# Kernel tuning notes

Measured on AMD Instinct MI355X. Metric: run time of the kernel, lower is better.

## Reference

```python
import jax, jax.numpy as jnp
import numpy as np

HEADS = 8
LN_EPS = 1e-5
BN_EPS = 1e-5
MIN_EPS, MAX_EPS = 1e-4, 10.0


def _ln(x, g, b):
    m = x.mean(-1, keepdims=True)
    v = x.var(-1, keepdims=True)
    return (x - m) / jnp.sqrt(v + LN_EPS) * g + b


def _pos2d(a, b, dim, temperature=10000.0):
    # faithful to build_2d_sincos_position_embedding(w=a, h=b)
    grid_a = jnp.arange(a, dtype=jnp.float32)
    grid_b = jnp.arange(b, dtype=jnp.float32)
    ga, gb = jnp.meshgrid(grid_a, grid_b, indexing='ij')  # (a, b)
    pos_dim = dim // 4
    omega = 1.0 / (temperature ** (jnp.arange(pos_dim, dtype=jnp.float32) / pos_dim))
    out_a = ga.flatten()[:, None] * omega[None]
    out_b = gb.flatten()[:, None] * omega[None]
    return jnp.concatenate([jnp.sin(out_a), jnp.cos(out_a), jnp.sin(out_b), jnp.cos(out_b)], axis=1)  # (a*b, dim)


def _avgpool(x, k):
    bb, cc, H, W = x.shape
    return x.reshape(bb, cc, H // k, k, W // k, k).mean((3, 5))


def setup_inputs() -> dict:
    key = jax.random.key(0)
    c1, c2, bs = 256, 512, 16
    ks = jax.random.split(key, 12)

    def lin(k, o, i):
        return (jax.random.normal(k, (o, i), jnp.float32) * (1.0 / np.sqrt(i))).astype(jnp.float32)

    return {
        'a3': jax.random.normal(ks[0], (bs, c1, 80, 80), jnp.float32),
        'a4': jax.random.normal(ks[1], (bs, c2, 40, 40), jnp.float32),
        'conv_w': lin(ks[2], c1, c2), 'conv_b': jnp.zeros((c1,), jnp.float32),
        'bn_g': jnp.ones((c1,), jnp.float32), 'bn_b': jnp.zeros((c1,), jnp.float32),
        'q_w': lin(ks[3], c1, c1), 'q_b': jnp.zeros((c1,), jnp.float32),
        'q_ln_g': jnp.ones((c1,), jnp.float32), 'q_ln_b': jnp.zeros((c1,), jnp.float32),
        'k_w': lin(ks[4], c1, c1), 'k_b': jnp.zeros((c1,), jnp.float32),
        'k_ln_g': jnp.ones((c1,), jnp.float32), 'k_ln_b': jnp.zeros((c1,), jnp.float32),
        'v_w': lin(ks[5], c1, c1), 'v_b': jnp.zeros((c1,), jnp.float32),
        'out_w': lin(ks[6], c1, c1), 'out_b': jnp.zeros((c1,), jnp.float32),
        'lin1_w': lin(ks[7], 4 * c1, c1), 'lin1_b': jnp.zeros((4 * c1,), jnp.float32),
        'lin2_w': lin(ks[8], c1, 4 * c1), 'lin2_b': jnp.zeros((c1,), jnp.float32),
        'norm1_g': jnp.ones((c1,), jnp.float32), 'norm1_b': jnp.zeros((c1,), jnp.float32),
        'norm2_g': jnp.ones((c1,), jnp.float32), 'norm2_b': jnp.zeros((c1,), jnp.float32),
        'idx': 10,
    }


def reference(a3, a4, conv_w, conv_b, bn_g, bn_b, q_w, q_b, q_ln_g, q_ln_b,
              k_w, k_b, k_ln_g, k_ln_b, v_w, v_b, out_w, out_b,
              lin1_w, lin1_b, lin2_w, lin2_b, norm1_g, norm1_b, norm2_g, norm2_b, idx):
    a3 = jnp.nan_to_num(a3, nan=0.0, posinf=1e4, neginf=-1e4)
    a4 = jnp.nan_to_num(a4, nan=0.0, posinf=1e4, neginf=-1e4)
    orig_a3, orig_a4 = a3, a4

    # high_to_low_embed: 1x1 conv + BatchNorm (eval: running_mean=0, running_var=1)
    a4e = jnp.einsum('bchw,oc->bohw', a4, conv_w) + conv_b[None, :, None, None]
    a4e = a4e / jnp.sqrt(1.0 + BN_EPS) * bn_g[None, :, None, None] + bn_b[None, :, None, None]

    if idx == 10:
        a3d = _avgpool(a3, 2)
    else:
        a3d = _avgpool(a3, 4)
        a4e = _avgpool(a4e, 2)

    bs, c, h, w = a3d.shape
    tgt = h * w
    src = a4e.shape[2] * a4e.shape[3]

    residual = a3d.reshape(bs, c, tgt).transpose(0, 2, 1)      # (bs, tgt, c)
    a3f = a3d.reshape(bs, c, tgt).transpose(2, 0, 1)            # (tgt, bs, c)
    a4f = a4e.reshape(bs, c, src).transpose(2, 0, 1)            # (src, bs, c)

    pos = _pos2d(h, w, c)[:, None, :]                           # (h*w, 1, c)
    a3f = a3f + pos
    a4f = a4f + pos                                             # src == tgt by construction

    Q = jax.nn.relu(_ln(a3f @ q_w.T + q_b, q_ln_g, q_ln_b))
    K = jax.nn.relu(_ln(a4f @ k_w.T + k_b, k_ln_g, k_ln_b))
    V = a4f @ v_w.T + v_b

    hd = c // HEADS
    Q = Q.reshape(tgt, bs, HEADS, hd).transpose(1, 2, 0, 3)     # (b, h, tgt, hd)
    K = K.reshape(src, bs, HEADS, hd).transpose(1, 2, 0, 3)
    V = V.reshape(src, bs, HEADS, hd).transpose(1, 2, 0, 3)

    m = max(src, tgt)
    wi = (np.pi / 2) * jnp.arange(1, m + 1, dtype=jnp.float32) / m  # (m,)
    sq = jnp.sin(wi[:tgt])[None, None, :, None]
    cq = jnp.cos(wi[:tgt])[None, None, :, None]
    sk = jnp.sin(wi[:src])[None, None, :, None]
    ck = jnp.cos(wi[:src])[None, None, :, None]
    Q_ = jnp.concatenate([Q * sq, Q * cq], -1)                  # (b, h, tgt, 2hd)
    K_ = jnp.concatenate([K * sk, K * ck], -1)                  # (b, h, src, 2hd)

    KV = jnp.einsum('bhsd,bhse->bhde', K_, V)                   # (b, h, 2hd, hd)
    Zden = jnp.einsum('bhld,bhd->bhl', Q_, K_.sum(2))
    Z = 1.0 / jnp.clip(Zden, MIN_EPS, MAX_EPS)
    attn = jnp.einsum('bhld,bhde->bhle', Q_, KV) * Z[..., None]  # (b, h, tgt, hd)

    attn = attn.transpose(2, 0, 1, 3).reshape(tgt, bs, c)
    out = (attn @ out_w.T + out_b).transpose(1, 0, 2)           # (bs, tgt, c)
    out = _ln(out, norm1_g, norm1_b)
    out = residual + out

    res2 = out
    ff = jax.nn.gelu(out @ lin1_w.T + lin1_b, approximate=False) @ lin2_w.T + lin2_b
    ff = _ln(ff, norm2_g, norm2_b)
    out = res2 + ff

    a3_sa = out.transpose(0, 2, 1).reshape(bs, c, h, w)
    a3_sa = jax.image.resize(a3_sa, orig_a3.shape, 'bilinear')  # align_corners=False
    a3_sa = a3_sa * orig_a3

    B4, C4, H4, W4 = orig_a4.shape
    a4_up = jax.image.resize(orig_a4, (B4, C4, 2 * H4, 2 * W4), 'bilinear')
    return (a3_sa, a4_up)
```

## Files before the change

### kernel.cpp

```cpp
#include <hip/hip_runtime.h>
#include <math.h>


typedef __attribute__((ext_vector_type(8))) short bf16x8;
typedef __attribute__((ext_vector_type(8))) unsigned short us8;
typedef __attribute__((ext_vector_type(4))) unsigned short us4h;
typedef __attribute__((ext_vector_type(4))) float f32x4;

__device__ __forceinline__ unsigned short f2bf(float f) {
  unsigned int u = __float_as_uint(f);
  u += 0x7fff + ((u >> 16) & 1);
  return (unsigned short)(u >> 16);
}
__device__ __forceinline__ float bf2f(unsigned short u) {
  return __uint_as_float(((unsigned int)u) << 16);
}

__device__ __forceinline__ void gload16(const void* g, void* l) {
  __builtin_amdgcn_global_load_lds(
      (const __attribute__((address_space(1))) void*)g,
      (__attribute__((address_space(3))) void*)l, 16, 0, 0);
}

__global__ __launch_bounds__(256) void prep_kernel(
    const float* __restrict__ cw, const float* __restrict__ qw,
    const float* __restrict__ kw, const float* __restrict__ vw,
    const float* __restrict__ ow, const float* __restrict__ l1w,
    const float* __restrict__ l2w, unsigned short* __restrict__ wbf,
    float* __restrict__ pos) {
  if (blockIdx.x < 448) {
    int gid = blockIdx.x * 256 + threadIdx.x;
    size_t e0 = (size_t)gid * 8;
    const float* src; size_t off;
    if (e0 < 131072)      { src = cw;  off = e0; }
    else if (e0 < 196608) { src = qw;  off = e0 - 131072; }
    else if (e0 < 262144) { src = kw;  off = e0 - 196608; }
    else if (e0 < 327680) { src = vw;  off = e0 - 262144; }
    else if (e0 < 393216) { src = ow;  off = e0 - 327680; }
    else if (e0 < 655360) { src = l1w; off = e0 - 393216; }
    else                  { src = l2w; off = e0 - 655360; }
    float4 v0 = *(const float4*)(src + off);
    float4 v1 = *(const float4*)(src + off + 4);
    us8 r;
    r[0] = f2bf(v0.x); r[1] = f2bf(v0.y); r[2] = f2bf(v0.z); r[3] = f2bf(v0.w);
    r[4] = f2bf(v1.x); r[5] = f2bf(v1.y); r[6] = f2bf(v1.z); r[7] = f2bf(v1.w);
    *(us8*)(wbf + e0) = r;
  } else {
    int s = blockIdx.x - 448, c = threadIdx.x;
    int y = s / 40, x = s - y * 40;
    int quad = c >> 6, i = c & 63;
    float omega = expf(-(float)i * (9.2103403719761836f / 64.0f));
    float coord = (quad < 2) ? (float)y : (float)x;
    float a = coord * omega;
    pos[s * 256 + c] = (quad & 1) ? cosf(a) : sinf(a);
  }
}

__global__ __launch_bounds__(640) void avgpool_kernel(
    const float* __restrict__ a3, const float* __restrict__ pos,
    unsigned short* __restrict__ X3) {
  __shared__ float buf2[256][44];
  int y = blockIdx.x, b = blockIdx.y;
  int tid = threadIdx.x;
  int x2 = tid % 20, cq = tid / 20;
#pragma unroll
  for (int it = 0; it < 8; ++it) {
    int c = cq + 32 * it;
    const float* p = a3 + (((size_t)(b * 256 + c) * 80 + 2 * y) * 80 + x2 * 4);
    float4 r0 = *(const float4*)p;
    float4 r1 = *(const float4*)(p + 80);
    buf2[c][2 * x2]     = 0.25f * ((r0.x + r0.y) + (r1.x + r1.y));
    buf2[c][2 * x2 + 1] = 0.25f * ((r0.z + r0.w) + (r1.z + r1.w));
  }
  __syncthreads();
  size_t t0 = (size_t)b * 1600 + y * 40;
  int sbase = y * 40;
#pragma unroll
  for (int it = 0; it < 4; ++it) {
    int idx = it * 640 + tid;
    int c = idx & 255, xq = idx >> 8;
    int x0 = xq * 4;
    float4 v = *(const float4*)&buf2[c][x0];
#pragma unroll
    for (int j = 0; j < 4; ++j) {
      float pv = pos[(size_t)(sbase + x0 + j) * 256 + c];
      float vv = (j == 0) ? v.x : (j == 1) ? v.y : (j == 2) ? v.z : v.w;
      X3[(t0 + x0 + j) * 256 + c] = f2bf(vv + pv);
    }
  }
}

__global__ __launch_bounds__(256) void a4t_kernel(
    const float* __restrict__ a4, unsigned short* __restrict__ a4t) {
  __shared__ float buf[64][65];
  int s0 = blockIdx.x * 64, k0 = blockIdx.y * 64, b = blockIdx.z;
  const float* src = a4 + ((size_t)b * 512 + k0) * 1600 + s0;
#pragma unroll
  for (int p = 0; p < 4; ++p) {
    int idx = p * 256 + threadIdx.x;
    int kk = idx >> 4, s4 = (idx & 15) * 4;
    float4 v = *(const float4*)(src + (size_t)kk * 1600 + s4);
    buf[kk][s4 + 0] = v.x; buf[kk][s4 + 1] = v.y;
    buf[kk][s4 + 2] = v.z; buf[kk][s4 + 3] = v.w;
  }
  __syncthreads();
  unsigned short* dst = a4t + ((size_t)b * 1600 + s0) * 512 + k0;
#pragma unroll
  for (int p = 0; p < 4; ++p) {
    int idx = p * 256 + threadIdx.x;
    int ss = idx >> 4, kq = (idx & 15) * 4;
    us4h v;
    v[0] = f2bf(buf[kq + 0][ss]); v[1] = f2bf(buf[kq + 1][ss]);
    v[2] = f2bf(buf[kq + 2][ss]); v[3] = f2bf(buf[kq + 3][ss]);
    *(us4h*)(dst + (size_t)ss * 512 + kq) = v;
  }
}

struct __align__(16) SmemT {
  unsigned short Albs[64][32];
  unsigned short Wlds[256][32];
  float part[4][64][2];
};

template<int EPI>
__device__ __forceinline__ void gemm_body(
    SmemT& S,
    const unsigned short* __restrict__ A, const unsigned short* __restrict__ W,
    const float* __restrict__ bias, void* __restrict__ outp,
    const int K, const int ldN, int t0, int o0,
    const float* __restrict__ posb,
    const float* __restrict__ g1, const float* __restrict__ b1,
    const unsigned short* __restrict__ res) {
  int tid = threadIdx.x;
  int lane = tid & 63, w = tid >> 6;
  int mw = w >> 2, nw = w & 3;
  int g = lane >> 4, cl = lane & 15;
  f32x4 acc[2][4] = {};

  int arow = lane >> 2, acol = (lane & 3) * 8;
  const unsigned short* ag  = A + (size_t)(t0 + (w & 3) * 16 + arow) * K + acol;
  const unsigned short* wgA = W + (size_t)(o0 + w * 16 + arow) * K + acol;
  const unsigned short* wgB = W + (size_t)(o0 + 128 + w * 16 + arow) * K + acol;
  unsigned short* al  = &S.Albs[(w & 3) * 16][0];
  unsigned short* wlA = &S.Wlds[w * 16][0];
  unsigned short* wlB = &S.Wlds[128 + w * 16][0];

  for (int k0 = 0; k0 < K; k0 += 32) {
    __syncthreads();
    if (w < 4) gload16(ag + k0, al);
    gload16(wgA + k0, wlA);
    gload16(wgB + k0, wlB);
    __syncthreads();
    bf16x8 af[2], bw[4];
#pragma unroll
    for (int ms = 0; ms < 2; ++ms)
      af[ms] = *(const bf16x8*)&S.Albs[mw * 32 + ms * 16 + cl][g * 8];
#pragma unroll
    for (int ns = 0; ns < 4; ++ns)
      bw[ns] = *(const bf16x8*)&S.Wlds[nw * 64 + ns * 16 + cl][g * 8];
#pragma unroll
    for (int ms = 0; ms < 2; ++ms)
#pragma unroll
      for (int ns = 0; ns < 4; ++ns)
        acc[ms][ns] = __builtin_amdgcn_mfma_f32_16x16x32_bf16(af[ms], bw[ns], acc[ms][ns], 0, 0, 0);
  }

  float bv[4];
#pragma unroll
  for (int ns = 0; ns < 4; ++ns) bv[ns] = bias[o0 + nw * 64 + ns * 16 + cl];
  int sbase = t0 % 1600;

  if constexpr (EPI == 2 || EPI == 3 || EPI == 5) {
#pragma unroll
    for (int ms = 0; ms < 2; ++ms) {
#pragma unroll
      for (int i = 0; i < 4; ++i) {
        float p = 0.f, q = 0.f;
#pragma unroll
        for (int ns = 0; ns < 4; ++ns) {
          float v = acc[ms][ns][i] + bv[ns];
          p += v; q += v * v;
        }
        p += __shfl_xor(p, 1); q += __shfl_xor(q, 1);
        p += __shfl_xor(p, 2); q += __shfl_xor(q, 2);
        p += __shfl_xor(p, 4); q += __shfl_xor(q, 4);
        p += __shfl_xor(p, 8); q += __shfl_xor(q, 8);
        if (cl == 0) {
          int rl = mw * 32 + ms * 16 + g * 4 + i;
          S.part[nw][rl][0] = p;
          S.part[nw][rl][1] = q;
        }
      }
    }
    __syncthreads();
  }

  if constexpr (EPI == 5) {
    float* of = (float*)outp;
    int bb = t0 / 1600;
#pragma unroll
    for (int ms = 0; ms < 2; ++ms) {
      int rl0 = mw * 32 + ms * 16 + g * 4;
      float mean[4], inv[4];
#pragma unroll
      for (int i = 0; i < 4; ++i) {
        float sp = (S.part[0][rl0 + i][0] + S.part[1][rl0 + i][0]) +
                   (S.part[2][rl0 + i][0] + S.part[3][rl0 + i][0]);
        float sq = (S.part[0][rl0 + i][1] + S.part[1][rl0 + i][1]) +
                   (S.part[2][rl0 + i][1] + S.part[3][rl0 + i][1]);
        mean[i] = sp * (1.f / 256.f);
        float var = sq * (1.f / 256.f) - mean[i] * mean[i];
        inv[i] = rsqrtf(var + 1e-5f);
      }
#pragma unroll
      for (int ns = 0; ns < 4; ++ns) {
        int col = nw * 64 + ns * 16 + cl;
        float gg = g1[col], b2 = b1[col];
        float4 y;
#pragma unroll
        for (int i = 0; i < 4; ++i) {
          float v = acc[ms][ns][i] + bv[ns];
          float yy = (v - mean[i]) * inv[i] * gg + b2;
          yy += bf2f(res[(size_t)(t0 + rl0 + i) * 256 + col]);
          if (i == 0) y.x = yy; else if (i == 1) y.y = yy;
          else if (i == 2) y.z = yy; else y.w = yy;
        }
        *(float4*)(of + ((size_t)(bb * 256 + col) * 1600) + sbase + rl0) = y;
      }
    }
    return;
  }

  unsigned short* ob = (unsigned short*)outp;
#pragma unroll
  for (int ms = 0; ms < 2; ++ms) {
#pragma unroll
    for (int i = 0; i < 4; ++i) {
      int rl = mw * 32 + ms * 16 + g * 4 + i;
      int t = t0 + rl;
      float mean = 0.f, inv = 0.f;
      if constexpr (EPI == 2 || EPI == 3) {
        float sp = (S.part[0][rl][0] + S.part[1][rl][0]) + (S.part[2][rl][0] + S.part[3][rl][0]);
        float sq = (S.part[0][rl][1] + S.part[1][rl][1]) + (S.part[2][rl][1] + S.part[3][rl][1]);
        mean = sp * (1.f / 256.f);
        float var = sq * (1.f / 256.f) - mean * mean;
        inv = rsqrtf(var + 1e-5f);
      }
#pragma unroll
      for (int ns = 0; ns < 4; ++ns) {
        int col = nw * 64 + ns * 16 + cl;
        float v = acc[ms][ns][i] + bv[ns];
        size_t oidx = (size_t)t * ldN + o0 + col;
        if constexpr (EPI == 0) {
          ob[oidx] = f2bf(v);
        } else if constexpr (EPI == 1) {
          const float is = 0.99999500003749968f;
          float y = v * (is * g1[col]) + b1[col] + posb[(size_t)(sbase + rl) * 256 + col];
          ob[oidx] = f2bf(y);
        } else if constexpr (EPI == 2) {
          float y = (v - mean) * inv * g1[col] + b1[col];
          ob[oidx] = f2bf(fmaxf(y, 0.f));
        } else if constexpr (EPI == 3) {
          float y = (v - mean) * inv * g1[col] + b1[col];
          y += bf2f(res[(size_t)t * 256 + col]) - posb[(size_t)(sbase + rl) * 256 + col];
          ob[oidx] = f2bf(y);
        } else if constexpr (EPI == 4) {
          float y = 0.5f * v * (1.f + erff(v * 0.7071067811865475f));
          ob[oidx] = f2bf(y);
        }
      }
    }
  }
}

template<int EPI>
__global__ __launch_bounds__(512) void fgemm(
    const unsigned short* __restrict__ A, const unsigned short* __restrict__ W,
    const float* __restrict__ bias, void* __restrict__ outp,
    const int K, const int ldN,
    const float* __restrict__ posb,
    const float* __restrict__ g1, const float* __restrict__ b1,
    const unsigned short* __restrict__ res) {
  __shared__ SmemT S;
  gemm_body<EPI>(S, A, W, bias, outp, K, ldN, blockIdx.x * 64, blockIdx.y * 256,
                 posb, g1, b1, res);
}

__global__ __launch_bounds__(512) void qkv_kernel(
    const unsigned short* __restrict__ X3b, const unsigned short* __restrict__ X4b,
    const unsigned short* __restrict__ w_q, const unsigned short* __restrict__ w_k,
    const unsigned short* __restrict__ w_v,
    const float* __restrict__ q_b, const float* __restrict__ k_b, const float* __restrict__ v_b,
    const float* __restrict__ q_g, const float* __restrict__ q_bt,
    const float* __restrict__ k_g, const float* __restrict__ k_bt,
    unsigned short* __restrict__ Qo, unsigned short* __restrict__ Ko,
    unsigned short* __restrict__ Vo) {
  __shared__ SmemT S;
  int t0 = blockIdx.x * 64;
  if (blockIdx.y == 0) {
    gemm_body<2>(S, X3b, w_q, q_b, Qo, 256, 256, t0, 0, nullptr, q_g, q_bt, nullptr);
  } else if (blockIdx.y == 1) {
    gemm_body<2>(S, X4b, w_k, k_b, Ko, 256, 256, t0, 0, nullptr, k_g, k_bt, nullptr);
  } else {
    gemm_body<0>(S, X4b, w_v, v_b, Vo, 256, 256, t0, 0, nullptr, nullptr, nullptr, nullptr);
  }
}

__global__ __launch_bounds__(256) void kv_kernel(
    const unsigned short* __restrict__ Kb, const unsigned short* __restrict__ Vb,
    float* __restrict__ KVp, float* __restrict__ Ksp) {
  __shared__ float Kc[64][32];
  __shared__ float Vc[64][32];
  __shared__ float sv[64], cv[64];
  __shared__ float red[4][64];
  int bx = blockIdx.x;
  int bh = bx / 5, sp = bx - bh * 5;
  int b = bh >> 3, h = bh & 7;
  int tid = threadIdx.x;
  int e = tid & 31, dg = tid >> 5;
  int d4 = dg * 4;
  int dks = tid & 63, partid = tid >> 6;
  float accs[4] = {0.f, 0.f, 0.f, 0.f};
  float accc[4] = {0.f, 0.f, 0.f, 0.f};
  float ks = 0.f;
  size_t base = ((size_t)b * 1600) * 256 + h * 32;
  for (int s0 = sp * 320; s0 < sp * 320 + 320; s0 += 64) {
    __syncthreads();
#pragma unroll
    for (int p = 0; p < 8; ++p) {
      int si = dg + p * 8;
      Kc[si][e] = bf2f(Kb[base + (size_t)(s0 + si) * 256 + e]);
      Vc[si][e] = bf2f(Vb[base + (size_t)(s0 + si) * 256 + e]);
    }
    if (tid < 64) {
      float wv = 1.5707963267948966f * (float)(s0 + tid + 1) * (1.0f / 1600.0f);
      sv[tid] = sinf(wv);
      cv[tid] = cosf(wv);
    }
    __syncthreads();
#pragma unroll 8
    for (int si = 0; si < 64; ++si) {
      float vv = Vc[si][e];
      float sn = sv[si], cs = cv[si];
      float4 k4 = *(const float4*)&Kc[si][d4];
      float p0 = k4.x * vv, p1 = k4.y * vv, p2 = k4.z * vv, p3 = k4.w * vv;
      accs[0] = fmaf(p0, sn, accs[0]); accc[0] = fmaf(p0, cs, accc[0]);
      accs[1] = fmaf(p1, sn, accs[1]); accc[1] = fmaf(p1, cs, accc[1]);
      accs[2] = fmaf(p2, sn, accs[2]); accc[2] = fmaf(p2, cs, accc[2]);
      accs[3] = fmaf(p3, sn, accs[3]); accc[3] = fmaf(p3, cs, accc[3]);
    }
#pragma unroll 4
    for (int q = 0; q < 16; ++q) {
      int si = partid * 16 + q;
      float kvv = (dks < 32) ? Kc[si][dks] * sv[si] : Kc[si][dks - 32] * cv[si];
      ks += kvv;
    }
  }
  red[partid][dks] = ks;
  __syncthreads();
  size_t ob = (size_t)sp * 128 + bh;
  if (tid < 64)
    Ksp[ob * 64 + tid] = (red[0][tid] + red[1][tid]) + (red[2][tid] + red[3][tid]);
#pragma unroll
  for (int i = 0; i < 4; ++i) {
    KVp[ob * 2048 + (d4 + i) * 32 + e] = accs[i];
    KVp[ob * 2048 + (32 + d4 + i) * 32 + e] = accc[i];
  }
}

__global__ __launch_bounds__(256) void kvred_kernel(
    const float* __restrict__ KVp, const float* __restrict__ Ksp,
    float* __restrict__ KV, float* __restrict__ Ks) {
  int bh = blockIdx.x, tid = threadIdx.x;
  size_t o = (size_t)bh * 2048 + tid * 8;
  float4 s0 = make_float4(0, 0, 0, 0), s1 = make_float4(0, 0, 0, 0);
#pragma unroll
  for (int sp = 0; sp < 5; ++sp) {
    const float* p = KVp + ((size_t)sp * 128 + bh) * 2048 + tid * 8;
    float4 a = *(const float4*)p;
    float4 b2 = *(const float4*)(p + 4);
    s0.x += a.x; s0.y += a.y; s0.z += a.z; s0.w += a.w;
    s1.x += b2.x; s1.y += b2.y; s1.z += b2.z; s1.w += b2.w;
  }
  *(float4*)(KV + o) = s0;
  *(float4*)(KV + o + 4) = s1;
  if (tid < 64) {
    float t = 0.f;
#pragma unroll
    for (int sp = 0; sp < 5; ++sp) t += Ksp[((size_t)sp * 128 + bh) * 64 + tid];
    Ks[bh * 64 + tid] = t;
  }
}

__global__ __launch_bounds__(256) void attn_kernel(
    const unsigned short* __restrict__ Qb, const float* __restrict__ KV,
    const float* __restrict__ Ksum, unsigned short* __restrict__ attn) {
  int grp = threadIdx.x >> 5;
  int e = threadIdx.x & 31;
  int t = blockIdx.x * 8 + grp;
  int b = t / 1600, s = t - b * 1600;
  float wv = 1.5707963267948966f * (float)(s + 1) * (1.0f / 1600.0f);
  float sq = sinf(wv), cq = cosf(wv);
  const unsigned short* qrow = Qb + (size_t)t * 256;
  for (int h = 0; h < 8; ++h) {
    int bh = b * 8 + h;
    const float* kv = KV + (size_t)bh * 2048;
    const float* ksm = Ksum + (size_t)bh * 64;
    float qe = bf2f(qrow[h * 32 + e]);
    float zp = qe * (sq * ksm[e] + cq * ksm[32 + e]);
    zp += __shfl_xor(zp, 1); zp += __shfl_xor(zp, 2);
    zp += __shfl_xor(zp, 4); zp += __shfl_xor(zp, 8); zp += __shfl_xor(zp, 16);
    float acc = 0.f;
#pragma unroll 8
    for (int d = 0; d < 32; ++d) {
      float qv = bf2f(qrow[h * 32 + d]);
      acc = fmaf(qv * sq, kv[d * 32 + e], acc);
      acc = fmaf(qv * cq, kv[(32 + d) * 32 + e], acc);
    }
    float zc = fminf(fmaxf(zp, 1e-4f), 10.0f);
    attn[(size_t)t * 256 + h * 32 + e] = f2bf(acc * (1.0f / zc));
  }
}

__device__ __forceinline__ float4 up_row4(const float* sm, int Y, int q) {
  float fy = Y * 0.5f - 0.25f;
  int iy = (int)floorf(fy);
  float dy = fy - (float)iy;
  int y0 = iy < 0 ? 0 : iy;
  int y1 = (iy + 1) > 39 ? 39 : (iy + 1);
  const float* r0 = sm + y0 * 40;
  const float* r1 = sm + y1 * 40;
  int cm1 = (2 * q - 1) < 0 ? 0 : (2 * q - 1);
  int cp2 = (2 * q + 2) > 39 ? 39 : (2 * q + 2);
  float w1 = 1.f - dy;
  float s0 = w1 * r0[cm1]       + dy * r1[cm1];
  float s1 = w1 * r0[2 * q]     + dy * r1[2 * q];
  float s2 = w1 * r0[2 * q + 1] + dy * r1[2 * q + 1];
  float s3 = w1 * r0[cp2]       + dy * r1[cp2];
  float4 o;
  o.x = 0.25f * s0 + 0.75f * s1;
  o.y = 0.75f * s1 + 0.25f * s2;
  o.z = 0.25f * s1 + 0.75f * s2;
  o.w = 0.75f * s2 + 0.25f * s3;
  return o;
}

__global__ __launch_bounds__(256) void upsample_fused_kernel(
    const float* __restrict__ a3p, const float* __restrict__ a3,
    const float* __restrict__ a4, float* __restrict__ out0,
    float* __restrict__ out1) {
  __shared__ float sm[1600];
  int id = blockIdx.x;
  const float* src;
  float* outp;
  const float* mul = nullptr;
  if (id < 4096) {
    int c = id & 255, b = id >> 8;
    src = a3p + ((size_t)b * 256 + c) * 1600;
    outp = out0 + ((size_t)b * 256 + c) * 6400;
    mul = a3 + ((size_t)b * 256 + c) * 6400;
  } else {
    int id2 = id - 4096;
    int c = id2 & 511, b = id2 >> 9;
    src = a4 + ((size_t)b * 512 + c) * 1600;
    outp = out1 + ((size_t)b * 512 + c) * 6400;
  }
  for (int i = threadIdx.x; i < 400; i += 256)
    *(float4*)&sm[i * 4] = *(const float4*)(src + i * 4);
  __syncthreads();
  if (mul) {
    for (int i = threadIdx.x; i < 1600; i += 256) {
      int Y = i / 20, q = i - Y * 20;
      float4 o = up_row4(sm, Y, q);
      float4 m = *(const float4*)(mul + i * 4);
      o.x *= m.x; o.y *= m.y; o.z *= m.z; o.w *= m.w;
      *(float4*)(outp + i * 4) = o;
    }
  } else {
    for (int i = threadIdx.x; i < 1600; i += 256) {
      int Y = i / 20, q = i - Y * 20;
      float4 o = up_row4(sm, Y, q);
      *(float4*)(outp + i * 4) = o;
    }
  }
}

extern "C" void kernel_launch(void* const* d_in, const int* in_sizes, int n_in,
                              void* d_out, int out_size, void* d_ws, size_t ws_size,
                              hipStream_t stream) {
  const float* a3     = (const float*)d_in[0];
  const float* a4     = (const float*)d_in[1];
  const float* conv_w = (const float*)d_in[2];
  const float* conv_b = (const float*)d_in[3];
  const float* bn_g   = (const float*)d_in[4];
  const float* bn_b   = (const float*)d_in[5];
  const float* q_w    = (const float*)d_in[6];
  const float* q_b    = (const float*)d_in[7];
  const float* q_ln_g = (const float*)d_in[8];
  const float* q_ln_b = (const float*)d_in[9];
  const float* k_w    = (const float*)d_in[10];
  const float* k_b    = (const float*)d_in[11];
  const float* k_ln_g = (const float*)d_in[12];
  const float* k_ln_b = (const float*)d_in[13];
  const float* v_w    = (const float*)d_in[14];
  const float* v_b    = (const float*)d_in[15];
  const float* out_w  = (const float*)d_in[16];
  const float* out_b  = (const float*)d_in[17];
  const float* lin1_w = (const float*)d_in[18];
  const float* lin1_b = (const float*)d_in[19];
  const float* lin2_w = (const float*)d_in[20];
  const float* lin2_b = (const float*)d_in[21];
  const float* n1_g   = (const float*)d_in[22];
  const float* n1_b   = (const float*)d_in[23];
  const float* n2_g   = (const float*)d_in[24];
  const float* n2_b   = (const float*)d_in[25];
  (void)in_sizes; (void)n_in; (void)out_size; (void)ws_size;

  float* ws = (float*)d_ws;
  float* pos  = ws + 0;
  unsigned short* wbf = (unsigned short*)(ws + 409600);
  float* KV   = ws + 868352;
  float* Ks   = ws + 1130496;
  float* KVp  = ws + 1138688;
  float* Ksp  = ws + 2449408;
  unsigned short* X3b  = (unsigned short*)(ws + 2490368);
  unsigned short* X4b  = (unsigned short*)(ws + 5767168);
  unsigned short* Qbb  = (unsigned short*)(ws + 9043968);
  unsigned short* Kbb  = (unsigned short*)(ws + 12320768);
  unsigned short* Vbb  = (unsigned short*)(ws + 15597568);
  unsigned short* o1b  = (unsigned short*)(ws + 18874368);
  unsigned short* a4tb = (unsigned short*)(ws + 22151168);
  unsigned short* ffhb = (unsigned short*)(ws + 22151168);
  float* a3p  = ws + 9043968;

  const unsigned short* w_conv = wbf;
  const unsigned short* w_q    = wbf + 131072;
  const unsigned short* w_k    = wbf + 196608;
  const unsigned short* w_v    = wbf + 262144;
  const unsigned short* w_o    = wbf + 327680;
  const unsigned short* w_l1   = wbf + 393216;
  const unsigned short* w_l2   = wbf + 655360;

  float* out0 = (float*)d_out;
  float* out1f = out0 + (size_t)16 * 256 * 80 * 80;

  prep_kernel<<<2048, 256, 0, stream>>>(conv_w, q_w, k_w, v_w, out_w, lin1_w, lin2_w, wbf, pos);
  avgpool_kernel<<<dim3(40, 16), 640, 0, stream>>>(a3, pos, X3b);
  a4t_kernel<<<dim3(25, 8, 16), 256, 0, stream>>>(a4, a4tb);
  fgemm<1><<<dim3(400, 1), 512, 0, stream>>>(a4tb, w_conv, conv_b, X4b, 512, 256, pos, bn_g, bn_b, nullptr);
  qkv_kernel<<<dim3(400, 3), 512, 0, stream>>>(X3b, X4b, w_q, w_k, w_v,
      q_b, k_b, v_b, q_ln_g, q_ln_b, k_ln_g, k_ln_b, Qbb, Kbb, Vbb);
  kv_kernel<<<640, 256, 0, stream>>>(Kbb, Vbb, KVp, Ksp);
  kvred_kernel<<<128, 256, 0, stream>>>(KVp, Ksp, KV, Ks);
  attn_kernel<<<3200, 256, 0, stream>>>(Qbb, KV, Ks, Kbb );
  fgemm<3><<<dim3(400, 1), 512, 0, stream>>>(Kbb, w_o, out_b, o1b, 256, 256, pos, n1_g, n1_b, X3b);
  fgemm<4><<<dim3(400, 4), 512, 0, stream>>>(o1b, w_l1, lin1_b, ffhb, 256, 1024, nullptr, nullptr, nullptr, nullptr);
  fgemm<5><<<dim3(400, 1), 512, 0, stream>>>(ffhb, w_l2, lin2_b, a3p, 1024, 256, nullptr, n2_g, n2_b, o1b);
  upsample_fused_kernel<<<12288, 256, 0, stream>>>(a3p, a3, a4, out0, out1f);
}
```

Baseline: 385.6 us.

## Merge a4 transpose into prep kernel and widen GEMM K-step to 64

The a4 transpose-to-bf16 work moves into the prep kernel as extra blocks, which removes one kernel launch. The shared GEMM body now loads a 64-wide K slab per iteration into two 32-wide LDS buffers, with all 8 waves sharing the loads. Each slab feeds two MFMA sub-steps, which halves the number of barrier pairs per tile. In exchange, LDS use per block doubles and the prep kernel now reserves a 64x65 float shared buffer on every block, which could lower occupancy.

```diff
diff --git a/kernel.cpp b/kernel.cpp
--- a/kernel.cpp
+++ b/kernel.cpp
@@ -27,7 +27,9 @@
     const float* __restrict__ kw, const float* __restrict__ vw,
     const float* __restrict__ ow, const float* __restrict__ l1w,
     const float* __restrict__ l2w, unsigned short* __restrict__ wbf,
-    float* __restrict__ pos) {
+    float* __restrict__ pos,
+    const float* __restrict__ a4, unsigned short* __restrict__ a4t) {
+  __shared__ float buf[64][65];
   if (blockIdx.x < 448) {
     int gid = blockIdx.x * 256 + threadIdx.x;
     size_t e0 = (size_t)gid * 8;
@@ -45,7 +47,7 @@
     r[0] = f2bf(v0.x); r[1] = f2bf(v0.y); r[2] = f2bf(v0.z); r[3] = f2bf(v0.w);
     r[4] = f2bf(v1.x); r[5] = f2bf(v1.y); r[6] = f2bf(v1.z); r[7] = f2bf(v1.w);
     *(us8*)(wbf + e0) = r;
-  } else {
+  } else if (blockIdx.x < 2048) {
     int s = blockIdx.x - 448, c = threadIdx.x;
     int y = s / 40, x = s - y * 40;
     int quad = c >> 6, i = c & 63;
@@ -53,6 +55,31 @@
     float coord = (quad < 2) ? (float)y : (float)x;
     float a = coord * omega;
     pos[s * 256 + c] = (quad & 1) ? cosf(a) : sinf(a);
+  } else {
+    int id = blockIdx.x - 2048;
+    int b = id / 200;
+    int r = id - b * 200;
+    int s0 = (r % 25) * 64, k0 = (r / 25) * 64;
+    const float* src = a4 + ((size_t)b * 512 + k0) * 1600 + s0;
+#pragma unroll
+    for (int p = 0; p < 4; ++p) {
+      int idx = p * 256 + threadIdx.x;
+      int kk = idx >> 4, s4 = (idx & 15) * 4;
+      float4 v = *(const float4*)(src + (size_t)kk * 1600 + s4);
+      buf[kk][s4 + 0] = v.x; buf[kk][s4 + 1] = v.y;
+      buf[kk][s4 + 2] = v.z; buf[kk][s4 + 3] = v.w;
+    }
+    __syncthreads();
+    unsigned short* dst = a4t + ((size_t)b * 1600 + s0) * 512 + k0;
+#pragma unroll
+    for (int p = 0; p < 4; ++p) {
+      int idx = p * 256 + threadIdx.x;
+      int ss = idx >> 4, kq = (idx & 15) * 4;
+      us4h v;
+      v[0] = f2bf(buf[kq + 0][ss]); v[1] = f2bf(buf[kq + 1][ss]);
+      v[2] = f2bf(buf[kq + 2][ss]); v[3] = f2bf(buf[kq + 3][ss]);
+      *(us4h*)(dst + (size_t)ss * 512 + kq) = v;
+    }
   }
 }
 
@@ -90,35 +117,9 @@
   }
 }
 
-__global__ __launch_bounds__(256) void a4t_kernel(
-    const float* __restrict__ a4, unsigned short* __restrict__ a4t) {
-  __shared__ float buf[64][65];
-  int s0 = blockIdx.x * 64, k0 = blockIdx.y * 64, b = blockIdx.z;
-  const float* src = a4 + ((size_t)b * 512 + k0) * 1600 + s0;
-#pragma unroll
-  for (int p = 0; p < 4; ++p) {
-    int idx = p * 256 + threadIdx.x;
-    int kk = idx >> 4, s4 = (idx & 15) * 4;
-    float4 v = *(const float4*)(src + (size_t)kk * 1600 + s4);
-    buf[kk][s4 + 0] = v.x; buf[kk][s4 + 1] = v.y;
-    buf[kk][s4 + 2] = v.z; buf[kk][s4 + 3] = v.w;
-  }
-  __syncthreads();
-  unsigned short* dst = a4t + ((size_t)b * 1600 + s0) * 512 + k0;
-#pragma unroll
-  for (int p = 0; p < 4; ++p) {
-    int idx = p * 256 + threadIdx.x;
-    int ss = idx >> 4, kq = (idx & 15) * 4;
-    us4h v;
-    v[0] = f2bf(buf[kq + 0][ss]); v[1] = f2bf(buf[kq + 1][ss]);
-    v[2] = f2bf(buf[kq + 2][ss]); v[3] = f2bf(buf[kq + 3][ss]);
-    *(us4h*)(dst + (size_t)ss * 512 + kq) = v;
-  }
-}
-
 struct __align__(16) SmemT {
-  unsigned short Albs[64][32];
-  unsigned short Wlds[256][32];
+  unsigned short Albs[2][64][32];
+  unsigned short Wlds[2][256][32];
   float part[4][64][2];
 };
 
@@ -137,32 +138,41 @@
   int g = lane >> 4, cl = lane & 15;
   f32x4 acc[2][4] = {};
 
-  int arow = lane >> 2, acol = (lane & 3) * 8;
-  const unsigned short* ag  = A + (size_t)(t0 + (w & 3) * 16 + arow) * K + acol;
-  const unsigned short* wgA = W + (size_t)(o0 + w * 16 + arow) * K + acol;
-  const unsigned short* wgB = W + (size_t)(o0 + 128 + w * 16 + arow) * K + acol;
-  unsigned short* al  = &S.Albs[(w & 3) * 16][0];
-  unsigned short* wlA = &S.Wlds[w * 16][0];
-  unsigned short* wlB = &S.Wlds[128 + w * 16][0];
-
-  for (int k0 = 0; k0 < K; k0 += 32) {
+  int lrow = lane >> 2, lchk = lane & 3;
+  const unsigned short* ag = A + (size_t)(t0 + (w >> 1) * 16 + lrow) * K
+                               + (w & 1) * 32 + lchk * 8;
+  unsigned short* al = &S.Albs[w & 1][(w >> 1) * 16][0];
+  const unsigned short* wg[4];
+  unsigned short* wl[4];
+#pragma unroll
+  for (int j = 0; j < 4; ++j) {
+    int u = w * 4 + j;
+    int kk = u & 1, rb = u >> 1;
+    wg[j] = W + (size_t)(o0 + rb * 16 + lrow) * K + kk * 32 + lchk * 8;
+    wl[j] = &S.Wlds[kk][rb * 16][0];
+  }
+
+  for (int k0 = 0; k0 < K; k0 += 64) {
     __syncthreads();
-    if (w < 4) gload16(ag + k0, al);
-    gload16(wgA + k0, wlA);
-    gload16(wgB + k0, wlB);
+    gload16(ag + k0, al);
+#pragma unroll
+    for (int j = 0; j < 4; ++j) gload16(wg[j] + k0, wl[j]);
     __syncthreads();
-    bf16x8 af[2], bw[4];
-#pragma unroll
-    for (int ms = 0; ms < 2; ++ms)
-      af[ms] = *(const bf16x8*)&S.Albs[mw * 32 + ms * 16 + cl][g * 8];
-#pragma unroll
-    for (int ns = 0; ns < 4; ++ns)
-      bw[ns] = *(const bf16x8*)&S.Wlds[nw * 64 + ns * 16 + cl][g * 8];
-#pragma unroll
-    for (int ms = 0; ms < 2; ++ms)
+#pragma unroll
+    for (int kk = 0; kk < 2; ++kk) {
+      bf16x8 af[2], bw[4];
+#pragma unroll
+      for (int ms = 0; ms < 2; ++ms)
+        af[ms] = *(const bf16x8*)&S.Albs[kk][mw * 32 + ms * 16 + cl][g * 8];
 #pragma unroll
       for (int ns = 0; ns < 4; ++ns)
-        acc[ms][ns] = __builtin_amdgcn_mfma_f32_16x16x32_bf16(af[ms], bw[ns], acc[ms][ns], 0, 0, 0);
+        bw[ns] = *(const bf16x8*)&S.Wlds[kk][nw * 64 + ns * 16 + cl][g * 8];
+#pragma unroll
+      for (int ms = 0; ms < 2; ++ms)
+#pragma unroll
+        for (int ns = 0; ns < 4; ++ns)
+          acc[ms][ns] = __builtin_amdgcn_mfma_f32_16x16x32_bf16(af[ms], bw[ns], acc[ms][ns], 0, 0, 0);
+    }
   }
 
   float bv[4];
@@ -544,9 +554,9 @@
   float* out0 = (float*)d_out;
   float* out1f = out0 + (size_t)16 * 256 * 80 * 80;
 
-  prep_kernel<<<2048, 256, 0, stream>>>(conv_w, q_w, k_w, v_w, out_w, lin1_w, lin2_w, wbf, pos);
+  prep_kernel<<<5248, 256, 0, stream>>>(conv_w, q_w, k_w, v_w, out_w, lin1_w, lin2_w,
+                                        wbf, pos, a4, a4tb);
   avgpool_kernel<<<dim3(40, 16), 640, 0, stream>>>(a3, pos, X3b);
-  a4t_kernel<<<dim3(25, 8, 16), 256, 0, stream>>>(a4, a4tb);
   fgemm<1><<<dim3(400, 1), 512, 0, stream>>>(a4tb, w_conv, conv_b, X4b, 512, 256, pos, bn_g, bn_b, nullptr);
   qkv_kernel<<<dim3(400, 3), 512, 0, stream>>>(X3b, X4b, w_q, w_k, w_v,
       q_b, k_b, v_b, q_ln_g, q_ln_b, k_ln_g, k_ln_b, Qbb, Kbb, Vbb);
```

After: 370.0 us. 4.1% less time.
